# Optimization experiments

Measured on AMD Instinct MI355X. Metric: run time of the kernel, lower is better.

The kernel has to match this reference:

```python
import jax, jax.numpy as jnp
import numpy as np

B, S, D, N = 8, 4096, 1024, 16
EPS = 1e-6


def setup_inputs() -> dict:
    key = jax.random.key(0)
    ks = jax.random.split(key, 6)
    s = 1.0 / np.sqrt(D)
    return {
        "x": jax.random.normal(ks[0], (B, S, D), dtype=jnp.float32),
        "W_lambda": jax.random.uniform(ks[1], (N, D), jnp.float32, -s, s),
        "b_lambda": jnp.full((N,), 2.0, dtype=jnp.float32),  # nn.init.constant_(bias, 2.0)
        "W_B": jax.random.uniform(ks[2], (N, D), jnp.float32, -s, s),
        "W_C": jax.random.uniform(ks[3], (D, N), jnp.float32, -1.0 / np.sqrt(N), 1.0 / np.sqrt(N)),
        "W_gate": jax.random.uniform(ks[4], (D, D), jnp.float32, -s, s),
        "rms_weight": jnp.ones((D,), dtype=jnp.float32),
    }


def reference(x, W_lambda, b_lambda, W_B, W_C, W_gate, rms_weight):
    # Input-dependent decay and input projection, computed for all timesteps at once
    lam = jax.nn.sigmoid(jnp.einsum("bsd,nd->bsn", x, W_lambda) + b_lambda)  # (B,S,N)
    Bx = jnp.einsum("bsd,nd->bsn", x, W_B)  # (B,S,N)

    def step(h, inp):
        l_t, b_t = inp
        h = l_t * h + b_t  # h_t = lambda_t * h_{t-1} + B_t x_t
        return h, h

    h0 = jnp.zeros((x.shape[0], W_B.shape[0]), dtype=x.dtype)
    _, hs = jax.lax.scan(step, h0, (jnp.swapaxes(lam, 0, 1), jnp.swapaxes(Bx, 0, 1)))
    hs = jnp.swapaxes(hs, 0, 1)  # (B,S,N)

    y = jnp.einsum("bsn,dn->bsd", hs, W_C)  # C @ h_t
    gate = jax.nn.sigmoid(jnp.einsum("bsd,ed->bse", x, W_gate))
    y = gate * y
    # RMSNorm
    rms = jax.lax.rsqrt(jnp.mean(y * y, axis=-1, keepdims=True) + EPS)
    return y * rms * rms_weight
```

## Files before the change

### kernel.cpp

```cpp
#include <hip/hip_runtime.h>

#define DD 1024
#define NN 16
#define SS 4096
#define BBATCH 8
#define TOK (BBATCH*SS)

typedef __attribute__((ext_vector_type(8))) __bf16 bf16x8;
typedef __attribute__((ext_vector_type(4))) __bf16 bf16x4;
typedef __attribute__((ext_vector_type(4))) float f32x4;
typedef unsigned int u32;
typedef unsigned long long u64;

__device__ __forceinline__ void async16(void* lds, const void* g) {
  __builtin_amdgcn_global_load_lds(
      (const __attribute__((address_space(1))) u32*)(u64)(g),
      (__attribute__((address_space(3))) u32*)(u32)(u64)(lds), 16, 0, 0);
}

__device__ __forceinline__ float sigmoidf_(float v) {
  return 1.f / (1.f + __expf(-v));
}

__global__ void k_cvtw(const float* __restrict__ wlf, const float* __restrict__ wbf,
                       __bf16* __restrict__ wp) {
  int i = blockIdx.x * blockDim.x + threadIdx.x;
  const int NP = NN * DD / 8;
  const float* src; __bf16* dst;
  if (i < NP)            { src = wlf + (u64)i * 8;            dst = wp + (u64)i * 8; }
  else if (i < 2 * NP)   { int j = i - NP; src = wbf + (u64)j * 8; dst = wp + NN * DD + (u64)j * 8; }
  else return;
  float4 a = *(const float4*)src, b = *(const float4*)(src + 4);
  bf16x8 o;
  o[0] = (__bf16)a.x; o[1] = (__bf16)a.y; o[2] = (__bf16)a.z; o[3] = (__bf16)a.w;
  o[4] = (__bf16)b.x; o[5] = (__bf16)b.y; o[6] = (__bf16)b.z; o[7] = (__bf16)b.w;
  *(bf16x8*)dst = o;
}

__global__ __launch_bounds__(256)
void k_proj(const float* __restrict__ x, const __bf16* __restrict__ wp,
            const float* __restrict__ b_lambda, __bf16* __restrict__ xb,
            float* __restrict__ lam, float* __restrict__ bx) {
  __shared__ __align__(16) __bf16 sA[32 * 32];
  __shared__ __align__(16) __bf16 sB[32 * 32];
  int tid = threadIdx.x;
  int lane = tid & 63, w = tid >> 6;
  int tok0 = blockIdx.x * 32;
  int r15 = lane & 15, kg = lane >> 4;
  int mt = w >> 1;
  int crow = tid >> 3, coff = (tid & 7) * 4;
  const float* xsrc = x + (u64)(tok0 + crow) * DD + coff;
  __bf16* xdst = xb + (u64)(tok0 + crow) * DD + coff;
  u32 aoff = (u32)crow * 64 +
             ((u32)((coff >> 3) ^ (crow & 3) ^ ((crow >> 2) & 3)) << 4) +
             ((coff & 4) ? 8u : 0u);
  u64 bSrc = 0;
  if (tid < 128) {
    int u = tid, row = u >> 2, slot = (u & 3) ^ (row & 3);
    bSrc = (u64)((const char*)wp + ((u64)row * DD + slot * 8) * 2);
  }
  f32x4 acc = {};
  int arow = mt * 16 + r15;
  u32 aro = (u32)arow * 64 + ((u32)(kg ^ (arow & 3) ^ ((arow >> 2) & 3)) << 4);
  int brow = (w & 1) * 16 + r15;
  u32 bro = (u32)brow * 64 + ((u32)(kg ^ (brow & 3)) << 4);
  for (int kt = 0; kt < DD / 32; ++kt) {
    float4 a0 = *(const float4*)(xsrc + kt * 32);
    bf16x4 cv;
    cv[0] = (__bf16)a0.x; cv[1] = (__bf16)a0.y; cv[2] = (__bf16)a0.z; cv[3] = (__bf16)a0.w;
    *(bf16x4*)(xdst + kt * 32) = cv;
    *(bf16x4*)((char*)sA + aoff) = cv;
    if (tid < 128)
      async16((char*)sB + (tid >> 6) * 1024, (const void*)(bSrc + kt * 64));
    __syncthreads();
    bf16x8 af = *(const bf16x8*)((const char*)sA + aro);
    bf16x8 bfr = *(const bf16x8*)((const char*)sB + bro);
    acc = __builtin_amdgcn_mfma_f32_16x16x32_bf16(af, bfr, acc, 0, 0, 0);
    __syncthreads();
  }
  float bl = b_lambda[r15];
#pragma unroll
  for (int r = 0; r < 4; ++r) {
    int token = tok0 + mt * 16 + kg * 4 + r;
    if ((w & 1) == 0) lam[token * NN + r15] = sigmoidf_(acc[r] + bl);
    else              bx[token * NN + r15] = acc[r];
  }
}

__global__ __launch_bounds__(256)
void k_scan(const float* __restrict__ lam, const float* __restrict__ bx,
            float* __restrict__ hs, const float* __restrict__ wgf,
            __bf16* __restrict__ wg) {
  if (blockIdx.x >= BBATCH * NN) {
    int i = (blockIdx.x - BBATCH * NN) * 256 + threadIdx.x;
    const float* src = wgf + (u64)i * 8;
    float4 a = *(const float4*)src, b = *(const float4*)(src + 4);
    bf16x8 o;
    o[0] = (__bf16)a.x; o[1] = (__bf16)a.y; o[2] = (__bf16)a.z; o[3] = (__bf16)a.w;
    o[4] = (__bf16)b.x; o[5] = (__bf16)b.y; o[6] = (__bf16)b.z; o[7] = (__bf16)b.w;
    *(bf16x8*)(wg + (u64)i * 8) = o;
    return;
  }
  int b = blockIdx.x >> 4, n = blockIdx.x & 15;
  int t = threadIdx.x;
  const int CH = SS / 256;
  float lv[CH], bv[CH];
  int base = (b * SS + t * CH) * NN + n;
  float a = 1.f, bacc = 0.f;
#pragma unroll
  for (int i = 0; i < CH; ++i) {
    lv[i] = lam[base + i * NN];
    bv[i] = bx[base + i * NN];
    bacc = lv[i] * bacc + bv[i];
    a *= lv[i];
  }
  __shared__ float As[2][256], Bs[2][256];
  As[0][t] = a; Bs[0][t] = bacc;
  __syncthreads();
  int cur = 0;
  for (int off = 1; off < 256; off <<= 1) {
    float a2 = As[cur][t], b2 = Bs[cur][t];
    if (t >= off) {
      float ap = As[cur][t - off], bp = Bs[cur][t - off];
      b2 = b2 + a2 * bp;
      a2 = a2 * ap;
    }
    As[cur ^ 1][t] = a2; Bs[cur ^ 1][t] = b2;
    cur ^= 1;
    __syncthreads();
  }
  float h = (t == 0) ? 0.f : Bs[cur][t - 1];
#pragma unroll
  for (int i = 0; i < CH; ++i) {
    h = lv[i] * h + bv[i];
    hs[base + i * NN] = h;
  }
}

#define STAGE(tile, M, h) do {                                                    \
    u32 lds0 = (u32)(((((tile) & 1) * 4 + (M) * 2 + (h)) << 14) + tid * 16);      \
    u64 g0 = ((M) ? bBase : aBase) + ((u64)(h) << 18) + (u64)(tile) * 128;        \
    async16(smc + lds0, (const void*)g0);                                         \
    async16(smc + lds0 + 8192, (const void*)(g0 + 131072));                       \
  } while (0)

template<int YB16>
__global__ __launch_bounds__(512, 2)
void k_gemm(const __bf16* __restrict__ xb, const __bf16* __restrict__ wg,
            const float* __restrict__ hs, const float* __restrict__ wc,
            float* __restrict__ outf, __bf16* __restrict__ outb) {
  __shared__ __align__(16) char smc[131072];
  const int tid = threadIdx.x, lane = tid & 63, w = tid >> 6;
  const int r15 = lane & 15, kg = lane >> 4;
  const int wr = w >> 2, wcq = w & 3;
  int bid = blockIdx.x;
  int swz = (bid & 7) * 64 + (bid >> 3);
  int m = swz >> 2, n = swz & 3;
  const int tok0 = m * 256, n0 = n * 256;
  const int sslot = (tid & 7) ^ ((tid >> 3) & 7);
  const u64 aBase = (u64)(const char*)xb + (u64)(tok0 + (tid >> 3)) * 2048 + (u32)sslot * 16;
  const u64 bBase = (u64)(const char*)wg + (u64)(n0 + (tid >> 3)) * 2048 + (u32)sslot * 16;
  const u32 sxa0 = (u32)(((0 | kg) ^ (r15 & 7)) * 16);
  const u32 sxa1 = (u32)(((4 | kg) ^ (r15 & 7)) * 16);
  const u32 lrB0 = (u32)((wcq & 1) * 64);

  f32x4 acc[8][4] = {};

  STAGE(0, 0, 0); STAGE(0, 0, 1); STAGE(0, 1, 0); STAGE(0, 1, 1);
  STAGE(1, 1, 0); STAGE(1, 1, 1); STAGE(1, 0, 0);
  asm volatile("s_waitcnt vmcnt(6)" ::: "memory");
  __builtin_amdgcn_s_barrier();
  asm volatile("" ::: "memory");

  for (int k = 0; k < 16; ++k) {
    const int b = k & 1;
    const char* Ah = smc + (u32)((b * 4 + wr) << 14);
    const char* Bh = smc + (u32)((b * 4 + 2 + (wcq >> 1)) << 14);
    bf16x8 af[8][2], bfr[4][2];
#pragma unroll
    for (int mt = 0; mt < 2; ++mt) {
      u32 ro = (u32)(mt * 16 + r15) * 128;
      af[mt][0] = *(const bf16x8*)(Ah + ro + sxa0);
      af[mt][1] = *(const bf16x8*)(Ah + ro + sxa1);
    }
#pragma unroll
    for (int nt = 0; nt < 4; ++nt) {
      u32 ro = (lrB0 + (u32)(nt * 16 + r15)) * 128;
      bfr[nt][0] = *(const bf16x8*)(Bh + ro + sxa0);
      bfr[nt][1] = *(const bf16x8*)(Bh + ro + sxa1);
    }
    if (k <= 14) STAGE(k + 1, 0, 1);
    __builtin_amdgcn_s_barrier();
    asm volatile("s_waitcnt lgkmcnt(0)" ::: "memory");
    __builtin_amdgcn_sched_barrier(0);
    __builtin_amdgcn_s_setprio(1);
#pragma unroll
    for (int mt = 0; mt < 2; ++mt)
#pragma unroll
      for (int nt = 0; nt < 4; ++nt) {
        acc[mt][nt] = __builtin_amdgcn_mfma_f32_16x16x32_bf16(af[mt][0], bfr[nt][0], acc[mt][nt], 0, 0, 0);
        acc[mt][nt] = __builtin_amdgcn_mfma_f32_16x16x32_bf16(af[mt][1], bfr[nt][1], acc[mt][nt], 0, 0, 0);
      }
    __builtin_amdgcn_s_setprio(0);
    __builtin_amdgcn_s_barrier();
    asm volatile("" ::: "memory");
#pragma unroll
    for (int mt = 2; mt < 6; ++mt) {
      u32 ro = (u32)(mt * 16 + r15) * 128;
      af[mt][0] = *(const bf16x8*)(Ah + ro + sxa0);
      af[mt][1] = *(const bf16x8*)(Ah + ro + sxa1);
    }
    if (k <= 13) STAGE(k + 2, 1, 0);
    __builtin_amdgcn_s_barrier();
    asm volatile("s_waitcnt lgkmcnt(0)" ::: "memory");
    __builtin_amdgcn_sched_barrier(0);
    __builtin_amdgcn_s_setprio(1);
#pragma unroll
    for (int mt = 2; mt < 4; ++mt)
#pragma unroll
      for (int nt = 0; nt < 4; ++nt) {
        acc[mt][nt] = __builtin_amdgcn_mfma_f32_16x16x32_bf16(af[mt][0], bfr[nt][0], acc[mt][nt], 0, 0, 0);
        acc[mt][nt] = __builtin_amdgcn_mfma_f32_16x16x32_bf16(af[mt][1], bfr[nt][1], acc[mt][nt], 0, 0, 0);
      }
    __builtin_amdgcn_s_setprio(0);
    __builtin_amdgcn_s_barrier();
    asm volatile("" ::: "memory");
#pragma unroll
    for (int mt = 6; mt < 8; ++mt) {
      u32 ro = (u32)(mt * 16 + r15) * 128;
      af[mt][0] = *(const bf16x8*)(Ah + ro + sxa0);
      af[mt][1] = *(const bf16x8*)(Ah + ro + sxa1);
    }
    if (k <= 13) STAGE(k + 2, 1, 1);
    __builtin_amdgcn_s_barrier();
    asm volatile("s_waitcnt lgkmcnt(0)" ::: "memory");
    __builtin_amdgcn_sched_barrier(0);
    __builtin_amdgcn_s_setprio(1);
#pragma unroll
    for (int mt = 4; mt < 6; ++mt)
#pragma unroll
      for (int nt = 0; nt < 4; ++nt) {
        acc[mt][nt] = __builtin_amdgcn_mfma_f32_16x16x32_bf16(af[mt][0], bfr[nt][0], acc[mt][nt], 0, 0, 0);
        acc[mt][nt] = __builtin_amdgcn_mfma_f32_16x16x32_bf16(af[mt][1], bfr[nt][1], acc[mt][nt], 0, 0, 0);
      }
    __builtin_amdgcn_s_setprio(0);
    __builtin_amdgcn_s_barrier();
    asm volatile("" ::: "memory");
    if (k <= 13) STAGE(k + 2, 0, 0);
    if (k <= 13)      asm volatile("s_waitcnt vmcnt(6)" ::: "memory");
    else if (k == 14) asm volatile("s_waitcnt vmcnt(0)" ::: "memory");
    __builtin_amdgcn_s_barrier();
    asm volatile("" ::: "memory");
    __builtin_amdgcn_s_setprio(1);
#pragma unroll
    for (int mt = 6; mt < 8; ++mt)
#pragma unroll
      for (int nt = 0; nt < 4; ++nt) {
        acc[mt][nt] = __builtin_amdgcn_mfma_f32_16x16x32_bf16(af[mt][0], bfr[nt][0], acc[mt][nt], 0, 0, 0);
        acc[mt][nt] = __builtin_amdgcn_mfma_f32_16x16x32_bf16(af[mt][1], bfr[nt][1], acc[mt][nt], 0, 0, 0);
      }
    __builtin_amdgcn_s_setprio(0);
  }
  asm volatile("" ::: "memory");

  __bf16* hsH = (__bf16*)smc;
  __bf16* hsL = (__bf16*)(smc + 16384);
  __bf16* wcB = (__bf16*)(smc + 32768);
  {
    int row = tid >> 1, half = tid & 1;
    const float* hp = hs + (u64)(tok0 + row) * NN + half * 8;
    const float* wp2 = wc + (u64)(n0 + row) * NN + half * 8;
    float4 h0 = *(const float4*)hp, h1 = *(const float4*)(hp + 4);
    float4 w0 = *(const float4*)wp2, w1 = *(const float4*)(wp2 + 4);
    bf16x8 hh, hl, wb, zz = {};
    float hv[8] = {h0.x, h0.y, h0.z, h0.w, h1.x, h1.y, h1.z, h1.w};
    float wv[8] = {w0.x, w0.y, w0.z, w0.w, w1.x, w1.y, w1.z, w1.w};
#pragma unroll
    for (int e = 0; e < 8; ++e) {
      __bf16 hi = (__bf16)hv[e];
      hh[e] = hi;
      hl[e] = (__bf16)(hv[e] - (float)hi);
      wb[e] = (__bf16)wv[e];
    }
    u32 realOff = (u32)row * 32 + (u32)((half ^ (row & 3)) << 3);
    u32 zeroOff = (u32)row * 32 + (u32)(((2 + half) ^ (row & 3)) << 3);
    *(bf16x8*)(hsH + realOff) = hh;  *(bf16x8*)(hsH + zeroOff) = zz;
    *(bf16x8*)(hsL + realOff) = hl;  *(bf16x8*)(hsL + zeroOff) = zz;
    *(bf16x8*)(wcB + realOff) = wb;  *(bf16x8*)(wcB + zeroOff) = zz;
  }
  __syncthreads();
  bf16x8 bw[4];
#pragma unroll
  for (int nt = 0; nt < 4; ++nt) {
    int row = wcq * 64 + nt * 16 + r15;
    bw[nt] = *(const bf16x8*)(wcB + row * 32 + ((kg ^ (row & 3)) << 3));
  }
  const f32x4 zero4 = {};
#pragma unroll
  for (int mt = 0; mt < 8; ++mt) {
    int arow = wr * 128 + mt * 16 + r15;
    u32 ao = (u32)arow * 32 + (u32)((kg ^ (arow & 3)) << 3);
    bf16x8 ah = *(const bf16x8*)(hsH + ao);
    bf16x8 al = *(const bf16x8*)(hsL + ao);
#pragma unroll
    for (int nt = 0; nt < 4; ++nt) {
      f32x4 cy4 = __builtin_amdgcn_mfma_f32_16x16x32_bf16(al, bw[nt], zero4, 0, 0, 0);
      cy4 = __builtin_amdgcn_mfma_f32_16x16x32_bf16(ah, bw[nt], cy4, 0, 0, 0);
      int j = wcq * 64 + nt * 16 + r15;
#pragma unroll
      for (int r = 0; r < 4; ++r) {
        int i = wr * 128 + mt * 16 + kg * 4 + r;
        float g = sigmoidf_(acc[mt][nt][r]);
        u64 off = (u64)(tok0 + i) * DD + n0 + j;
        if (YB16) outb[off] = (__bf16)(g * cy4[r]);
        else      outf[off] = g * cy4[r];
      }
    }
  }
}

__global__ __launch_bounds__(256)
void k_norm_b(const __bf16* __restrict__ yb, float* __restrict__ out,
              const float* __restrict__ rw) {
  int row = blockIdx.x * 4 + (threadIdx.x >> 6);
  int lane = threadIdx.x & 63;
  const __bf16* yrow = yb + (u64)row * DD;
  bf16x4 v[4];
  float f[16];
  float rs = 0.f;
#pragma unroll
  for (int q = 0; q < 4; ++q) {
    v[q] = *(const bf16x4*)(yrow + q * 256 + lane * 4);
#pragma unroll
    for (int e = 0; e < 4; ++e) {
      f[q * 4 + e] = (float)v[q][e];
      rs += f[q * 4 + e] * f[q * 4 + e];
    }
  }
#pragma unroll
  for (int msk = 1; msk < 64; msk <<= 1) rs += __shfl_xor(rs, msk, 64);
  float rstd = rsqrtf(rs * (1.f / DD) + 1e-6f);
  float* orow = out + (u64)row * DD;
#pragma unroll
  for (int q = 0; q < 4; ++q) {
    float4 wv = *(const float4*)(rw + q * 256 + lane * 4);
    float4 o;
    o.x = f[q * 4 + 0] * rstd * wv.x;
    o.y = f[q * 4 + 1] * rstd * wv.y;
    o.z = f[q * 4 + 2] * rstd * wv.z;
    o.w = f[q * 4 + 3] * rstd * wv.w;
    *(float4*)(orow + q * 256 + lane * 4) = o;
  }
}

__global__ __launch_bounds__(256)
void k_norm_f(float* __restrict__ out, const float* __restrict__ rw) {
  int row = blockIdx.x * 4 + (threadIdx.x >> 6);
  int lane = threadIdx.x & 63;
  float4* p = (float4*)(out + (u64)row * DD);
  float4 v[4];
  float rs = 0.f;
#pragma unroll
  for (int e = 0; e < 4; ++e) {
    v[e] = p[e * 64 + lane];
    rs += v[e].x * v[e].x + v[e].y * v[e].y + v[e].z * v[e].z + v[e].w * v[e].w;
  }
#pragma unroll
  for (int msk = 1; msk < 64; msk <<= 1) rs += __shfl_xor(rs, msk, 64);
  float rstd = rsqrtf(rs * (1.f / DD) + 1e-6f);
  const float4* rwp = (const float4*)rw;
#pragma unroll
  for (int e = 0; e < 4; ++e) {
    float4 wv = rwp[e * 64 + lane];
    float4 o;
    o.x = v[e].x * rstd * wv.x;
    o.y = v[e].y * rstd * wv.y;
    o.z = v[e].z * rstd * wv.z;
    o.w = v[e].w * rstd * wv.w;
    p[e * 64 + lane] = o;
  }
}

extern "C" void kernel_launch(void* const* d_in, const int* in_sizes, int n_in,
                              void* d_out, int out_size, void* d_ws, size_t ws_size,
                              hipStream_t stream) {
  (void)in_sizes; (void)n_in; (void)out_size;
  const float* x        = (const float*)d_in[0];
  const float* W_lambda = (const float*)d_in[1];
  const float* b_lambda = (const float*)d_in[2];
  const float* W_B      = (const float*)d_in[3];
  const float* W_C      = (const float*)d_in[4];
  const float* W_gate   = (const float*)d_in[5];
  const float* rms_w    = (const float*)d_in[6];
  char* ws = (char*)d_ws;
  __bf16* xb  = (__bf16*)(ws + 0);
  __bf16* wg  = (__bf16*)(ws + 67108864);
  __bf16* wp  = (__bf16*)(ws + 69206016);
  float*  lam = (float*)(ws + 69271552);
  float*  bx  = (float*)(ws + 71368704);
  float*  hs  = (float*)(ws + 73465856);
  __bf16* yb  = (__bf16*)(ws + 75563008);
  float*  out = (float*)d_out;
  bool yb16 = ws_size >= (size_t)(75563008ull + 67108864ull);

  k_cvtw<<<(2 * NN * DD / 8 + 255) / 256, 256, 0, stream>>>(W_lambda, W_B, wp);
  k_proj<<<TOK / 32, 256, 0, stream>>>(x, wp, b_lambda, xb, lam, bx);
  k_scan<<<BBATCH * NN + DD * DD / 8 / 256, 256, 0, stream>>>(lam, bx, hs, W_gate, wg);
  if (yb16) {
    k_gemm<1><<<(TOK / 256) * (DD / 256), 512, 0, stream>>>(xb, wg, hs, W_C, nullptr, yb);
    k_norm_b<<<TOK / 4, 256, 0, stream>>>(yb, out, rms_w);
  } else {
    k_gemm<0><<<(TOK / 256) * (DD / 256), 512, 0, stream>>>(xb, wg, hs, W_C, out, nullptr);
    k_norm_f<<<TOK / 4, 256, 0, stream>>>(out, rms_w);
  }
}
```

Measured before the change: 189.2 us.

## Enlarge projection tile to 128 tokens, fuse weight conversion, prefetch x

The projection kernel now handles 128 tokens per 512-thread block instead of 32. Each wave computes both the lambda and B projections from one shared A fragment, so the weight tile is loaded once per 128 tokens rather than once per 32. The separate fp32-to-bf16 weight conversion kernel is removed: weights are read as fp32 and converted in-kernel while being stored to LDS. A register double-buffer prefetches the next k-slice of x and the weights, to hide global latency behind the MFMA work. The trade-off is fewer blocks (256) and more registers per thread.

```diff
diff --git a/kernel.cpp b/kernel.cpp
--- a/kernel.cpp
+++ b/kernel.cpp
@@ -22,68 +22,73 @@
   return 1.f / (1.f + __expf(-v));
 }
 
-__global__ void k_cvtw(const float* __restrict__ wlf, const float* __restrict__ wbf,
-                       __bf16* __restrict__ wp) {
-  int i = blockIdx.x * blockDim.x + threadIdx.x;
-  const int NP = NN * DD / 8;
-  const float* src; __bf16* dst;
-  if (i < NP)            { src = wlf + (u64)i * 8;            dst = wp + (u64)i * 8; }
-  else if (i < 2 * NP)   { int j = i - NP; src = wbf + (u64)j * 8; dst = wp + NN * DD + (u64)j * 8; }
-  else return;
-  float4 a = *(const float4*)src, b = *(const float4*)(src + 4);
-  bf16x8 o;
-  o[0] = (__bf16)a.x; o[1] = (__bf16)a.y; o[2] = (__bf16)a.z; o[3] = (__bf16)a.w;
-  o[4] = (__bf16)b.x; o[5] = (__bf16)b.y; o[6] = (__bf16)b.z; o[7] = (__bf16)b.w;
-  *(bf16x8*)dst = o;
-}
-
-__global__ __launch_bounds__(256)
-void k_proj(const float* __restrict__ x, const __bf16* __restrict__ wp,
-            const float* __restrict__ b_lambda, __bf16* __restrict__ xb,
-            float* __restrict__ lam, float* __restrict__ bx) {
-  __shared__ __align__(16) __bf16 sA[32 * 32];
+__global__ __launch_bounds__(512)
+void k_proj(const float* __restrict__ x, const float* __restrict__ wlf,
+            const float* __restrict__ wbf, const float* __restrict__ b_lambda,
+            __bf16* __restrict__ xb, float* __restrict__ lam, float* __restrict__ bx) {
+  __shared__ __align__(16) __bf16 sA[128 * 32];
   __shared__ __align__(16) __bf16 sB[32 * 32];
   int tid = threadIdx.x;
   int lane = tid & 63, w = tid >> 6;
-  int tok0 = blockIdx.x * 32;
+  int tok0 = blockIdx.x * 128;
   int r15 = lane & 15, kg = lane >> 4;
-  int mt = w >> 1;
-  int crow = tid >> 3, coff = (tid & 7) * 4;
-  const float* xsrc = x + (u64)(tok0 + crow) * DD + coff;
-  __bf16* xdst = xb + (u64)(tok0 + crow) * DD + coff;
-  u32 aoff = (u32)crow * 64 +
-             ((u32)((coff >> 3) ^ (crow & 3) ^ ((crow >> 2) & 3)) << 4) +
-             ((coff & 4) ? 8u : 0u);
-  u64 bSrc = 0;
+  int crow = tid >> 2, cg = tid & 3;
+  const float* xsrc = x + (u64)(tok0 + crow) * DD + cg * 8;
+  __bf16* xdst = xb + (u64)(tok0 + crow) * DD + cg * 8;
+  u32 aoff = (u32)crow * 64 + ((u32)(cg ^ (crow & 3) ^ ((crow >> 2) & 3)) << 4);
+  const float* wsrc = nullptr;
+  u32 boff = 0;
   if (tid < 128) {
-    int u = tid, row = u >> 2, slot = (u & 3) ^ (row & 3);
-    bSrc = (u64)((const char*)wp + ((u64)row * DD + slot * 8) * 2);
-  }
-  f32x4 acc = {};
-  int arow = mt * 16 + r15;
+    int wrow = tid >> 2, wcg = tid & 3;
+    wsrc = (wrow < 16 ? wlf + (u64)wrow * DD : wbf + (u64)(wrow - 16) * DD) + wcg * 8;
+    boff = (u32)wrow * 64 + ((u32)(wcg ^ (wrow & 3)) << 4);
+  }
+  int arow = w * 16 + r15;
   u32 aro = (u32)arow * 64 + ((u32)(kg ^ (arow & 3) ^ ((arow >> 2) & 3)) << 4);
-  int brow = (w & 1) * 16 + r15;
-  u32 bro = (u32)brow * 64 + ((u32)(kg ^ (brow & 3)) << 4);
-  for (int kt = 0; kt < DD / 32; ++kt) {
-    float4 a0 = *(const float4*)(xsrc + kt * 32);
-    bf16x4 cv;
-    cv[0] = (__bf16)a0.x; cv[1] = (__bf16)a0.y; cv[2] = (__bf16)a0.z; cv[3] = (__bf16)a0.w;
-    *(bf16x4*)(xdst + kt * 32) = cv;
-    *(bf16x4*)((char*)sA + aoff) = cv;
-    if (tid < 128)
-      async16((char*)sB + (tid >> 6) * 1024, (const void*)(bSrc + kt * 64));
+  u32 bro0 = (u32)r15 * 64 + ((u32)(kg ^ (r15 & 3)) << 4);
+  int brow1 = 16 + r15;
+  u32 bro1 = (u32)brow1 * 64 + ((u32)(kg ^ (brow1 & 3)) << 4);
+  f32x4 acc0 = {}, acc1 = {};
+  float4 cx0 = *(const float4*)(xsrc);
+  float4 cx1 = *(const float4*)(xsrc + 4);
+  float4 cw0 = {}, cw1 = {};
+  if (tid < 128) { cw0 = *(const float4*)(wsrc); cw1 = *(const float4*)(wsrc + 4); }
+  for (int kt = 0; kt < 32; ++kt) {
+    float4 nx0, nx1, nw0 = {}, nw1 = {};
+    if (kt < 31) {
+      nx0 = *(const float4*)(xsrc + (kt + 1) * 32);
+      nx1 = *(const float4*)(xsrc + (kt + 1) * 32 + 4);
+      if (tid < 128) {
+        nw0 = *(const float4*)(wsrc + (kt + 1) * 32);
+        nw1 = *(const float4*)(wsrc + (kt + 1) * 32 + 4);
+      }
+    }
+    bf16x8 cv;
+    cv[0] = (__bf16)cx0.x; cv[1] = (__bf16)cx0.y; cv[2] = (__bf16)cx0.z; cv[3] = (__bf16)cx0.w;
+    cv[4] = (__bf16)cx1.x; cv[5] = (__bf16)cx1.y; cv[6] = (__bf16)cx1.z; cv[7] = (__bf16)cx1.w;
+    *(bf16x8*)(xdst + kt * 32) = cv;
+    *(bf16x8*)((char*)sA + aoff) = cv;
+    if (tid < 128) {
+      bf16x8 wv;
+      wv[0] = (__bf16)cw0.x; wv[1] = (__bf16)cw0.y; wv[2] = (__bf16)cw0.z; wv[3] = (__bf16)cw0.w;
+      wv[4] = (__bf16)cw1.x; wv[5] = (__bf16)cw1.y; wv[6] = (__bf16)cw1.z; wv[7] = (__bf16)cw1.w;
+      *(bf16x8*)((char*)sB + boff) = wv;
+    }
     __syncthreads();
     bf16x8 af = *(const bf16x8*)((const char*)sA + aro);
-    bf16x8 bfr = *(const bf16x8*)((const char*)sB + bro);
-    acc = __builtin_amdgcn_mfma_f32_16x16x32_bf16(af, bfr, acc, 0, 0, 0);
+    bf16x8 b0 = *(const bf16x8*)((const char*)sB + bro0);
+    bf16x8 b1 = *(const bf16x8*)((const char*)sB + bro1);
+    acc0 = __builtin_amdgcn_mfma_f32_16x16x32_bf16(af, b0, acc0, 0, 0, 0);
+    acc1 = __builtin_amdgcn_mfma_f32_16x16x32_bf16(af, b1, acc1, 0, 0, 0);
     __syncthreads();
+    if (kt < 31) { cx0 = nx0; cx1 = nx1; cw0 = nw0; cw1 = nw1; }
   }
   float bl = b_lambda[r15];
 #pragma unroll
   for (int r = 0; r < 4; ++r) {
-    int token = tok0 + mt * 16 + kg * 4 + r;
-    if ((w & 1) == 0) lam[token * NN + r15] = sigmoidf_(acc[r] + bl);
-    else              bx[token * NN + r15] = acc[r];
+    int token = tok0 + w * 16 + kg * 4 + r;
+    lam[token * NN + r15] = sigmoidf_(acc0[r] + bl);
+    bx[token * NN + r15] = acc1[r];
   }
 }
 
@@ -395,7 +400,6 @@
   char* ws = (char*)d_ws;
   __bf16* xb  = (__bf16*)(ws + 0);
   __bf16* wg  = (__bf16*)(ws + 67108864);
-  __bf16* wp  = (__bf16*)(ws + 69206016);
   float*  lam = (float*)(ws + 69271552);
   float*  bx  = (float*)(ws + 71368704);
   float*  hs  = (float*)(ws + 73465856);
@@ -403,8 +407,7 @@
   float*  out = (float*)d_out;
   bool yb16 = ws_size >= (size_t)(75563008ull + 67108864ull);
 
-  k_cvtw<<<(2 * NN * DD / 8 + 255) / 256, 256, 0, stream>>>(W_lambda, W_B, wp);
-  k_proj<<<TOK / 32, 256, 0, stream>>>(x, wp, b_lambda, xb, lam, bx);
+  k_proj<<<TOK / 128, 512, 0, stream>>>(x, W_lambda, W_B, b_lambda, xb, lam, bx);
   k_scan<<<BBATCH * NN + DD * DD / 8 / 256, 256, 0, stream>>>(lam, bx, hs, W_gate, wg);
   if (yb16) {
     k_gemm<1><<<(TOK / 256) * (DD / 256), 512, 0, stream>>>(xb, wg, hs, W_C, nullptr, yb);
```

Measured after the change: 184.9 us. 2.3% less time.
